# Performance work log

Hardware: AMD Instinct MI355X
Metric: run time of the kernel (lower is better)

## Reference

```python
import jax, jax.numpy as jnp
import numpy as np

N_QUBITS = 6
N_SHARED_LAYERS = 3
N_TASK_LAYERS = 2
ENC_HIDDEN = 256
INPUT_DIM = 784
BATCH = 256
P1Q = 0.001  # 1-qubit depolarizing prob
P2Q = 0.01   # 2-qubit-gate depolarizing approximation (applied as 1q channel, as in source)

C = jnp.complex64
PX = jnp.array([[0, 1], [1, 0]], C)
PY = jnp.array([[0, -1j], [1j, 0]], C)
PZ = jnp.array([[1, 0], [0, -1]], C)
CNOT = jnp.array([[1, 0, 0, 0], [0, 1, 0, 0], [0, 0, 0, 1], [0, 0, 1, 0]], C)

_LOW = 'abcdefghijklmnopqrstuvwxyz'


def _apply(dm, G, axes, batched):
    # contract gate G (rows=out, cols=in) into dm along absolute dm axes `axes`
    k = len(axes)
    G = G.reshape(G.shape[:G.ndim - 2] + (2,) * (2 * k))
    nd = dm.ndim - 1  # 2 * n_qubits
    dm_sub = ['Z'] + list(_LOW[:nd])
    out_sub = list(dm_sub)
    new = 'ABCD'
    gout, gin = [], []
    for j, ax in enumerate(axes):
        gout.append(new[j]); gin.append(dm_sub[ax]); out_sub[ax] = new[j]
    g_str = ('Z' if batched else '') + ''.join(gout) + ''.join(gin)
    return jnp.einsum(f"{g_str},{''.join(dm_sub)}->{''.join(out_sub)}", G, dm)


def apply_unitary(dm, U, wires, n, batched=False):
    # rho -> U rho U^dagger; ket axes are 1+w, bra axes 1+n+w
    dm = _apply(dm, U, [1 + w for w in wires], batched)
    return _apply(dm, jnp.conj(U), [1 + n + w for w in wires], batched)


def depolarize(dm, p, q, n):
    x = apply_unitary(dm, PX, [q], n)
    y = apply_unitary(dm, PY, [q], n)
    z = apply_unitary(dm, PZ, [q], n)
    return (1.0 - p) * dm + (p / 3.0) * (x + y + z)


def rot_mat(phi, theta, omega):
    # PennyLane Rot(phi, theta, omega) = RZ(omega) RY(theta) RZ(phi)
    c = jnp.cos(theta / 2)
    s = jnp.sin(theta / 2)
    ep = jnp.exp(-0.5j * (phi + omega))  # e^{-i(phi+omega)/2}
    em = jnp.exp(0.5j * (phi - omega))   # e^{+i(phi-omega)/2}
    return jnp.stack([jnp.stack([ep * c, -em * s]),
                      jnp.stack([jnp.conj(em) * s, jnp.conj(ep) * c])]).astype(C)


def ry_batched(theta):
    # theta: (B,) -> (B,2,2)
    c = jnp.cos(theta / 2)
    s = jnp.sin(theta / 2)
    return jnp.stack([jnp.stack([c, -s], -1),
                      jnp.stack([s, c], -1)], -2).astype(C)


def strongly_entangling(dm, w, n):
    # PennyLane StronglyEntanglingLayers, default ranges r = (l % (n-1)) + 1, CNOT ring
    L = w.shape[0]
    for l in range(L):
        for i in range(n):
            dm = apply_unitary(dm, rot_mat(w[l, i, 0], w[l, i, 1], w[l, i, 2]), [i], n)
        r = (l % (n - 1)) + 1
        for i in range(n):
            dm = apply_unitary(dm, CNOT, [i, (i + r) % n], n)
    return dm


def circuit(z, shared_w, task_w):
    n = N_QUBITS
    Bz = z.shape[0]
    dm = jnp.zeros((Bz,) + (2,) * (2 * n), C).at[(slice(None),) + (0,) * (2 * n)].set(1.0)
    for i in range(n):
        dm = apply_unitary(dm, ry_batched(z[:, i] * jnp.pi), [i], n, batched=True)
        dm = depolarize(dm, P1Q, i, n)
    dm = strongly_entangling(dm, shared_w, n)
    for i in range(n):
        dm = depolarize(dm, P1Q, i, n)
    for i in range(n - 1):
        dm = depolarize(dm, P2Q, i, n)
    dm = strongly_entangling(dm, task_w, n)
    for i in range(n):
        dm = depolarize(dm, P1Q, i, n)
    D = 2 ** n
    probs = jnp.real(jnp.diagonal(dm.reshape(Bz, D, D), axis1=1, axis2=2))  # (B, D)
    bits = (jnp.arange(D)[:, None] >> jnp.arange(n - 1, -1, -1)[None, :]) & 1  # wire 0 = MSB
    signs = (1 - 2 * bits).astype(jnp.float32)  # (D, n)
    return probs.astype(jnp.float32) @ signs    # (B, n) = <Z_i>


def setup_inputs():
    key = jax.random.key(0)
    ks = jax.random.split(key, 8)
    f = jnp.float32
    return {
        "x": jax.random.normal(ks[0], (BATCH, INPUT_DIM), f),
        "W1": jax.random.normal(ks[1], (ENC_HIDDEN, INPUT_DIM), f) * 0.03,
        "b1": jnp.zeros((ENC_HIDDEN,), f),
        "ln_g": jnp.ones((ENC_HIDDEN,), f),
        "ln_b": jnp.zeros((ENC_HIDDEN,), f),
        "W2": jax.random.normal(ks[2], (N_QUBITS, ENC_HIDDEN), f) * 0.05,
        "b2": jnp.zeros((N_QUBITS,), f),
        "shared_w": jax.random.normal(ks[3], (N_SHARED_LAYERS, N_QUBITS, 3), f) * 0.1,
        "task_w": jax.random.normal(ks[4], (N_TASK_LAYERS, N_QUBITS, 3), f) * 0.1,
        "Wp": jax.random.normal(ks[5], (2, N_QUBITS), f) * 0.1,
        "bp": jnp.zeros((2,), f),
    }


def reference(x, W1, b1, ln_g, ln_b, W2, b2, shared_w, task_w, Wp, bp):
    # encoder: Linear -> ReLU -> LayerNorm -> Linear -> Tanh
    h = jnp.maximum(x @ W1.T + b1, 0.0)
    mu = h.mean(-1, keepdims=True)
    var = ((h - mu) ** 2).mean(-1, keepdims=True)
    h = (h - mu) / jnp.sqrt(var + 1e-5) * ln_g + ln_b
    z = jnp.tanh(h @ W2.T + b2)            # (B, N_QUBITS)
    ev = circuit(z, shared_w, task_w)      # (B, N_QUBITS)
    return ev @ Wp.T + bp                  # (B, 2)
```

## Files before the change

### kernel.cpp

```cpp
#include <hip/hip_runtime.h>
#include <math.h>

#define NQ 6
#define BLK 1024
#define HID 256
#define INDIM 784
#define KC 56
#define NSPLIT 14

#define PW1 0.001f
#define PW2 0.01f
constexpr float WO1 = 1.f - 4.f * PW1 / 3.f;
constexpr float WO2 = 1.f - 4.f * PW2 / 3.f;
constexpr float WOc = WO1 * WO2;

struct alignas(16) RingTabs { int t[3][4096]; };
constexpr RingTabs make_ring_tabs() {
    RingTabs R{};
    for (int ri = 0; ri < 3; ++ri) {
        int r = ri + 1;
        for (int v = 0; v < 4096; ++v) {
            int x[6], z[6];
            for (int w = 0; w < 6; ++w) { x[w] = (v >> (2 * w + 1)) & 1; z[w] = (v >> (2 * w)) & 1; }
            int sgn = 0;
            for (int i = 5; i >= 0; --i) {
                int c = i, tg = (i + r) % 6;
                sgn ^= x[c] & z[tg] & (x[tg] ^ z[c] ^ 1);
                x[tg] ^= x[c];
                z[c]  ^= z[tg];
            }
            int s = 0;
            for (int w = 0; w < 6; ++w) s |= (x[w] << (2 * w + 1)) | (z[w] << (2 * w));
            R.t[ri][v] = s | (sgn << 31);
        }
    }
    return R;
}
static __device__ const RingTabs RT = make_ring_tabs();

__device__ __forceinline__ int swz(int n) {
    return n ^ ((((n >> 6) ^ (n >> 10)) & 3) << 3);
}

template<int CTRL>
__device__ __forceinline__ float qb(float v) {
    int r = __builtin_amdgcn_update_dpp(0, __builtin_bit_cast(int, v), CTRL, 0xF, 0xF, true);
    return __builtin_bit_cast(float, r);
}
template<int OFF>
__device__ __forceinline__ float swzl(float v) {
    return __builtin_bit_cast(float, __builtin_amdgcn_ds_swizzle(__builtin_bit_cast(int, v), OFF));
}

__device__ __forceinline__ void rot_reg(float e[4], float4 rZ, float4 rX, float4 rY) {
    float X = e[2], Y = e[3], Z = e[1];
    e[2] = fmaf(rX.x, X, fmaf(rX.y, Y, rX.z * Z));
    e[3] = fmaf(rY.x, X, fmaf(rY.y, Y, rY.z * Z));
    e[1] = fmaf(rZ.x, X, fmaf(rZ.y, Y, rZ.z * Z));
}
__device__ __forceinline__ void rot_q1(float e[4], float4 cf) {
    #pragma unroll
    for (int j = 0; j < 4; ++j) {
        float vZ = qb<0x55>(e[j]);
        float vX = qb<0xAA>(e[j]);
        float vY = qb<0xFF>(e[j]);
        e[j] = fmaf(cf.x, vX, fmaf(cf.y, vY, fmaf(cf.z, vZ, cf.w * e[j])));
    }
}
__device__ __forceinline__ void rot_q2(float e[4], float4 cf) {
    #pragma unroll
    for (int j = 0; j < 4; ++j) {
        float vZ = swzl<0x093>(e[j]);
        float vX = swzl<0x113>(e[j]);
        float vY = swzl<0x193>(e[j]);
        e[j] = fmaf(cf.x, vX, fmaf(cf.y, vY, fmaf(cf.z, vZ, cf.w * e[j])));
    }
}
__device__ __forceinline__ void rot_q3(float e[4], float4 cf, int lane) {
    int s1 = (lane & 15) | 16, s2 = (lane & 15) | 32, s3 = (lane & 15) | 48;
    #pragma unroll
    for (int j = 0; j < 4; ++j) {
        float vZ = __shfl(e[j], s1, 64);
        float vX = __shfl(e[j], s2, 64);
        float vY = __shfl(e[j], s3, 64);
        e[j] = fmaf(cf.x, vX, fmaf(cf.y, vY, fmaf(cf.z, vZ, cf.w * e[j])));
    }
}

__global__ __launch_bounds__(256)
void enc_gemm(const float* __restrict__ x, const float* __restrict__ W1,
              float* __restrict__ hp)
{
    __shared__ float xsT[KC][64];
    __shared__ float wsT[KC][64];
    const int tid = threadIdx.x;
    const int bid = blockIdx.x;
    const int tile = bid / NSPLIT;
    const int s = bid - tile * NSPLIT;
    const int bb = (tile >> 2) * 64;
    const int bu = (tile & 3) * 64;
    const int k0 = s * KC;

    for (int i = tid; i < 1792; i += 256) {
        int r = i & 63;
        int cb = i >> 6;
        int m = (cb >= 14);
        int c = cb - m * 14;
        const float* src = m ? (W1 + (size_t)(bu + r) * INDIM + k0 + 4 * c)
                             : (x  + (size_t)(bb + r) * INDIM + k0 + 4 * c);
        float4 v = *(const float4*)src;
        float (*dst)[64] = m ? wsT : xsT;
        dst[4 * c + 0][r] = v.x;
        dst[4 * c + 1][r] = v.y;
        dst[4 * c + 2][r] = v.z;
        dst[4 * c + 3][r] = v.w;
    }
    __syncthreads();

    const int tx = tid & 15, ty = tid >> 4;
    float acc[4][4] = {};
    #pragma unroll 7
    for (int k = 0; k < KC; ++k) {
        float4 xv = *(const float4*)&xsT[k][4 * ty];
        float4 wv = *(const float4*)&wsT[k][4 * tx];
        const float xa[4] = {xv.x, xv.y, xv.z, xv.w};
        const float wa[4] = {wv.x, wv.y, wv.z, wv.w};
        #pragma unroll
        for (int i = 0; i < 4; ++i)
            #pragma unroll
            for (int j = 0; j < 4; ++j)
                acc[i][j] = fmaf(xa[i], wa[j], acc[i][j]);
    }
    float* o = hp + (size_t)s * 65536 + (size_t)(bb + 4 * ty) * 256 + bu + 4 * tx;
    #pragma unroll
    for (int i = 0; i < 4; ++i)
        *(float4*)(o + (size_t)i * 256) = make_float4(acc[i][0], acc[i][1], acc[i][2], acc[i][3]);
}

__global__ __launch_bounds__(BLK)
void nqm_kernel(const float* __restrict__ hp, const float* __restrict__ b1,
                const float* __restrict__ ln_g, const float* __restrict__ ln_b,
                const float* __restrict__ W2, const float* __restrict__ b2,
                const float* __restrict__ shared_w, const float* __restrict__ task_w,
                const float* __restrict__ Wp, const float* __restrict__ bp,
                float* __restrict__ out)
{
    __shared__ __align__(16) float dmA[4096];
    __shared__ __align__(16) float dmB[4096];
    __shared__ __align__(16) float4 Mlane[30][4];
    __shared__ float bloch[NQ][4];
    __shared__ float red[4], red2[4];
    __shared__ float zpart[4][8];
    __shared__ float bcast[2];
    __shared__ float evs[8];

    const int tid = threadIdx.x;
    const int b = blockIdx.x;
    const int wv = tid >> 6;
    const int lane = tid & 63;

    float h = 0.0f;
    if (tid < 256) {
        const float* hb = hp + (size_t)b * 256 + tid;
        h = b1[tid];
        #pragma unroll
        for (int s = 0; s < NSPLIT; ++s) h += hb[(size_t)s * 65536];
        h = fmaxf(h, 0.0f);
        float s = h, s2 = h * h;
        #pragma unroll
        for (int off = 32; off > 0; off >>= 1) {
            s  += __shfl_down(s, off, 64);
            s2 += __shfl_down(s2, off, 64);
        }
        if (lane == 0) { red[tid >> 6] = s; red2[tid >> 6] = s2; }
    }
    __syncthreads();
    if (tid == 0) {
        float ts  = red[0] + red[1] + red[2] + red[3];
        float ts2 = red2[0] + red2[1] + red2[2] + red2[3];
        float mu  = ts * (1.0f / HID);
        float var = ts2 * (1.0f / HID) - mu * mu;
        bcast[0] = mu;
        bcast[1] = rsqrtf(var + 1e-5f);
    }
    __syncthreads();
    if (tid < 256) {
        float hnj = (h - bcast[0]) * bcast[1] * ln_g[tid] + ln_b[tid];
        float p[NQ];
        #pragma unroll
        for (int i = 0; i < NQ; ++i) p[i] = hnj * W2[i * HID + tid];
        #pragma unroll
        for (int off = 32; off > 0; off >>= 1) {
            #pragma unroll
            for (int i = 0; i < NQ; ++i) p[i] += __shfl_down(p[i], off, 64);
        }
        if (lane == 0) {
            #pragma unroll
            for (int i = 0; i < NQ; ++i) zpart[tid >> 6][i] = p[i];
        }
    }
    __syncthreads();

    if (tid < NQ) {
        float z = zpart[0][tid] + zpart[1][tid] + zpart[2][tid] + zpart[3][tid] + b2[tid];
        z = tanhf(z);
        float sn, c;
        sincosf(z * 3.14159265358979323846f, &sn, &c);
        bloch[tid][0] = 1.0f;
        bloch[tid][1] = WO1 * c;
        bloch[tid][2] = WO1 * sn;
        bloch[tid][3] = 0.0f;
    } else if (tid < 36) {
        int g = tid - NQ;
        int layer = g / NQ;
        int wire = g % NQ;
        const float* w = (layer < 3) ? (shared_w + (layer * NQ + wire) * 3)
                                     : (task_w + ((layer - 3) * NQ + wire) * 3);
        float phi = w[0], theta = w[1], omega = w[2];
        float sf, cf_, st, ct, so, co;
        sincosf(phi, &sf, &cf_);
        sincosf(theta, &st, &ct);
        sincosf(omega, &so, &co);
        float M00 = co * ct * cf_ - so * sf;
        float M01 = -co * ct * sf - so * cf_;
        float M02 = co * st;
        float M10 = so * ct * cf_ + co * sf;
        float M11 = -so * ct * sf + co * cf_;
        float M12 = so * st;
        float M20 = -st * cf_;
        float M21 = st * sf;
        float M22 = ct;
        float f = (layer == 3) ? ((wire < 5) ? WOc : WO1) : 1.0f;
        Mlane[g][0] = make_float4(0.f, 0.f, 0.f, 1.f);
        Mlane[g][1] = make_float4(f * M20, f * M21, f * M22, 0.f);
        Mlane[g][2] = make_float4(f * M00, f * M01, f * M02, 0.f);
        Mlane[g][3] = make_float4(f * M10, f * M11, f * M12, 0.f);
    }

    const int q1 = lane & 3, q2 = (lane >> 2) & 3, q3 = (lane >> 4) & 3;
    const int q4 = wv & 3, q5 = wv >> 2;
    const int baseB = ((lane & 3) << 10) | (wv << 4) | (lane >> 2);
    const int rtab[4] = {0, 1, 2, 0};
    __syncthreads();

    for (int l = 0; l < 5; ++l) {
        const int g0 = l * 6;
        float e[4];

        if (l == 0) {
            float A = bloch[1][q1] * bloch[2][q2] * bloch[3][q3] * bloch[4][q4] * bloch[5][q5];
            e[0] = A * bloch[0][0];
            e[1] = A * bloch[0][1];
            e[2] = A * bloch[0][2];
            e[3] = A * bloch[0][3];
        } else {
            const int4 te = *(const int4*)&RT.t[rtab[l - 1]][tid << 2];
            float v0 = dmA[swz(te.x & 4095)];
            float v1 = dmA[swz(te.y & 4095)];
            float v2 = dmA[swz(te.z & 4095)];
            float v3 = dmA[swz(te.w & 4095)];
            e[0] = __int_as_float(__float_as_int(v0) ^ (te.x & 0x80000000));
            e[1] = __int_as_float(__float_as_int(v1) ^ (te.y & 0x80000000));
            e[2] = __int_as_float(__float_as_int(v2) ^ (te.z & 0x80000000));
            e[3] = __int_as_float(__float_as_int(v3) ^ (te.w & 0x80000000));
        }
        rot_reg(e, Mlane[g0 + 0][1], Mlane[g0 + 0][2], Mlane[g0 + 0][3]);
        rot_q1(e, Mlane[g0 + 1][q1]);
        rot_q2(e, Mlane[g0 + 2][q2]);
        rot_q3(e, Mlane[g0 + 3][q3], lane);
        *(float4*)&dmB[swz(tid << 2)] = make_float4(e[0], e[1], e[2], e[3]);
        __syncthreads();

        e[0] = dmB[swz(baseB)];
        e[1] = dmB[swz(baseB + 256)];
        e[2] = dmB[swz(baseB + 512)];
        e[3] = dmB[swz(baseB + 768)];
        rot_reg(e, Mlane[g0 + 4][1], Mlane[g0 + 4][2], Mlane[g0 + 4][3]);
        rot_q1(e, Mlane[g0 + 5][lane & 3]);
        dmA[swz(baseB)]       = e[0];
        dmA[swz(baseB + 256)] = e[1];
        dmA[swz(baseB + 512)] = e[2];
        dmA[swz(baseB + 768)] = e[3];
        __syncthreads();
    }

    if (tid < NQ) {
        int e = RT.t[1][1 << (2 * tid)];
        float v = dmA[swz(e & 4095)];
        v = __int_as_float(__float_as_int(v) ^ (e & 0x80000000));
        evs[tid] = WO1 * v;
    }
    __syncthreads();
    if (tid < 2) {
        float o = bp[tid];
        #pragma unroll
        for (int i = 0; i < NQ; ++i) o = fmaf(evs[i], Wp[tid * NQ + i], o);
        out[b * 2 + tid] = o;
    }
}

extern "C" void kernel_launch(void* const* d_in, const int* in_sizes, int n_in,
                              void* d_out, int out_size, void* d_ws, size_t ws_size,
                              hipStream_t stream) {
    (void)in_sizes; (void)n_in; (void)ws_size; (void)out_size;
    const float* x        = (const float*)d_in[0];
    const float* W1       = (const float*)d_in[1];
    const float* b1       = (const float*)d_in[2];
    const float* ln_g     = (const float*)d_in[3];
    const float* ln_b     = (const float*)d_in[4];
    const float* W2       = (const float*)d_in[5];
    const float* b2       = (const float*)d_in[6];
    const float* shared_w = (const float*)d_in[7];
    const float* task_w   = (const float*)d_in[8];
    const float* Wp       = (const float*)d_in[9];
    const float* bp       = (const float*)d_in[10];
    float* out = (float*)d_out;
    float* hp  = (float*)d_ws;

    hipLaunchKernelGGL(enc_gemm, dim3(16 * NSPLIT), dim3(256), 0, stream, x, W1, hp);
    hipLaunchKernelGGL(nqm_kernel, dim3(256), dim3(BLK), 0, stream,
                       hp, b1, ln_g, ln_b, W2, b2, shared_w, task_w, Wp, bp, out);
}
```

Baseline: 95.25 us.

## Fuse encoder GEMM and circuit kernels into one cooperative launch with grid sync

Merges the split-K encoder GEMM and the density-matrix circuit kernel into a single cooperative kernel of 256 blocks of 1024 threads. The first 224 blocks compute the GEMM partials with a 2x2 per-thread tile, then a grid-wide sync orders them before the circuit phase. Shared memory is overlapped through a union. The swizzle is also folded into the constexpr ring tables, saving runtime index math. This removes one kernel launch and its inter-kernel gap, but adds grid-sync cost, a lower-ILP GEMM tile, and needs all 256 large blocks to be co-resident.

```diff
diff --git a/kernel.cpp b/kernel.cpp
--- a/kernel.cpp
+++ b/kernel.cpp
@@ -1,5 +1,8 @@
 #include <hip/hip_runtime.h>
+#include <hip/hip_cooperative_groups.h>
 #include <math.h>
+
+namespace cg = cooperative_groups;
 
 #define NQ 6
 #define BLK 1024
@@ -13,6 +16,13 @@
 constexpr float WO1 = 1.f - 4.f * PW1 / 3.f;
 constexpr float WO2 = 1.f - 4.f * PW2 / 3.f;
 constexpr float WOc = WO1 * WO2;
+
+constexpr int cswz(int n) {
+    return n ^ ((((n >> 6) ^ (n >> 10)) & 3) << 3);
+}
+__device__ __forceinline__ int swz(int n) {
+    return n ^ ((((n >> 6) ^ (n >> 10)) & 3) << 3);
+}
 
 struct alignas(16) RingTabs { int t[3][4096]; };
 constexpr RingTabs make_ring_tabs() {
@@ -31,16 +41,12 @@
             }
             int s = 0;
             for (int w = 0; w < 6; ++w) s |= (x[w] << (2 * w + 1)) | (z[w] << (2 * w));
-            R.t[ri][v] = s | (sgn << 31);
+            R.t[ri][v] = cswz(s) | (sgn << 31);
         }
     }
     return R;
 }
 static __device__ const RingTabs RT = make_ring_tabs();
-
-__device__ __forceinline__ int swz(int n) {
-    return n ^ ((((n >> 6) ^ (n >> 10)) & 3) << 3);
-}
 
 template<int CTRL>
 __device__ __forceinline__ float qb(float v) {
@@ -87,78 +93,79 @@
     }
 }
 
-__global__ __launch_bounds__(256)
-void enc_gemm(const float* __restrict__ x, const float* __restrict__ W1,
-              float* __restrict__ hp)
+union SharedU {
+    struct {
+        float xsT[KC][64];
+        float wsT[KC][64];
+    } g;
+    struct {
+        alignas(16) float dmA[4096];
+        alignas(16) float dmB[4096];
+        alignas(16) float4 Mlane[30][4];
+        float bloch[NQ][4];
+        float red[4], red2[4];
+        float zpart[4][8];
+        float bcast[2];
+        float evs[8];
+    } c;
+};
+
+__global__ __launch_bounds__(BLK)
+void fused_k(const float* __restrict__ x, const float* __restrict__ W1,
+             const float* __restrict__ b1, const float* __restrict__ ln_g,
+             const float* __restrict__ ln_b, const float* __restrict__ W2,
+             const float* __restrict__ b2, const float* __restrict__ shared_w,
+             const float* __restrict__ task_w, const float* __restrict__ Wp,
+             const float* __restrict__ bp, float* __restrict__ out,
+             float* __restrict__ hp)
 {
-    __shared__ float xsT[KC][64];
-    __shared__ float wsT[KC][64];
-    const int tid = threadIdx.x;
-    const int bid = blockIdx.x;
-    const int tile = bid / NSPLIT;
-    const int s = bid - tile * NSPLIT;
-    const int bb = (tile >> 2) * 64;
-    const int bu = (tile & 3) * 64;
-    const int k0 = s * KC;
-
-    for (int i = tid; i < 1792; i += 256) {
-        int r = i & 63;
-        int cb = i >> 6;
-        int m = (cb >= 14);
-        int c = cb - m * 14;
-        const float* src = m ? (W1 + (size_t)(bu + r) * INDIM + k0 + 4 * c)
-                             : (x  + (size_t)(bb + r) * INDIM + k0 + 4 * c);
-        float4 v = *(const float4*)src;
-        float (*dst)[64] = m ? wsT : xsT;
-        dst[4 * c + 0][r] = v.x;
-        dst[4 * c + 1][r] = v.y;
-        dst[4 * c + 2][r] = v.z;
-        dst[4 * c + 3][r] = v.w;
-    }
-    __syncthreads();
-
-    const int tx = tid & 15, ty = tid >> 4;
-    float acc[4][4] = {};
-    #pragma unroll 7
-    for (int k = 0; k < KC; ++k) {
-        float4 xv = *(const float4*)&xsT[k][4 * ty];
-        float4 wv = *(const float4*)&wsT[k][4 * tx];
-        const float xa[4] = {xv.x, xv.y, xv.z, xv.w};
-        const float wa[4] = {wv.x, wv.y, wv.z, wv.w};
-        #pragma unroll
-        for (int i = 0; i < 4; ++i)
-            #pragma unroll
-            for (int j = 0; j < 4; ++j)
-                acc[i][j] = fmaf(xa[i], wa[j], acc[i][j]);
-    }
-    float* o = hp + (size_t)s * 65536 + (size_t)(bb + 4 * ty) * 256 + bu + 4 * tx;
-    #pragma unroll
-    for (int i = 0; i < 4; ++i)
-        *(float4*)(o + (size_t)i * 256) = make_float4(acc[i][0], acc[i][1], acc[i][2], acc[i][3]);
-}
-
-__global__ __launch_bounds__(BLK)
-void nqm_kernel(const float* __restrict__ hp, const float* __restrict__ b1,
-                const float* __restrict__ ln_g, const float* __restrict__ ln_b,
-                const float* __restrict__ W2, const float* __restrict__ b2,
-                const float* __restrict__ shared_w, const float* __restrict__ task_w,
-                const float* __restrict__ Wp, const float* __restrict__ bp,
-                float* __restrict__ out)
-{
-    __shared__ __align__(16) float dmA[4096];
-    __shared__ __align__(16) float dmB[4096];
-    __shared__ __align__(16) float4 Mlane[30][4];
-    __shared__ float bloch[NQ][4];
-    __shared__ float red[4], red2[4];
-    __shared__ float zpart[4][8];
-    __shared__ float bcast[2];
-    __shared__ float evs[8];
-
+    __shared__ SharedU su;
     const int tid = threadIdx.x;
     const int b = blockIdx.x;
     const int wv = tid >> 6;
     const int lane = tid & 63;
 
+    if (b < 16 * NSPLIT) {
+        const int tile = b / NSPLIT;
+        const int s = b - tile * NSPLIT;
+        const int bb = (tile >> 2) * 64;
+        const int bu = (tile & 3) * 64;
+        const int k0 = s * KC;
+
+        for (int i = tid; i < 1792; i += BLK) {
+            int r = i & 63;
+            int cb = i >> 6;
+            int m = (cb >= 14);
+            int c = cb - m * 14;
+            const float* src = m ? (W1 + (size_t)(bu + r) * INDIM + k0 + 4 * c)
+                                 : (x  + (size_t)(bb + r) * INDIM + k0 + 4 * c);
+            float4 v = *(const float4*)src;
+            float (*dst)[64] = m ? su.g.wsT : su.g.xsT;
+            dst[4 * c + 0][r] = v.x;
+            dst[4 * c + 1][r] = v.y;
+            dst[4 * c + 2][r] = v.z;
+            dst[4 * c + 3][r] = v.w;
+        }
+        __syncthreads();
+
+        const int tx = tid & 31, ty = tid >> 5;
+        float a00 = 0.f, a01 = 0.f, a10 = 0.f, a11 = 0.f;
+        #pragma unroll 7
+        for (int k = 0; k < KC; ++k) {
+            float2 xv = *(const float2*)&su.g.xsT[k][2 * ty];
+            float2 wvv = *(const float2*)&su.g.wsT[k][2 * tx];
+            a00 = fmaf(xv.x, wvv.x, a00);
+            a01 = fmaf(xv.x, wvv.y, a01);
+            a10 = fmaf(xv.y, wvv.x, a10);
+            a11 = fmaf(xv.y, wvv.y, a11);
+        }
+        float* o = hp + (size_t)s * 65536 + (size_t)(bb + 2 * ty) * 256 + bu + 2 * tx;
+        o[0] = a00; o[1] = a01;
+        o[256] = a10; o[257] = a11;
+    }
+
+    cg::this_grid().sync();
+
     float h = 0.0f;
     if (tid < 256) {
         const float* hb = hp + (size_t)b * 256 + tid;
@@ -172,20 +179,20 @@
             s  += __shfl_down(s, off, 64);
             s2 += __shfl_down(s2, off, 64);
         }
-        if (lane == 0) { red[tid >> 6] = s; red2[tid >> 6] = s2; }
+        if (lane == 0) { su.c.red[tid >> 6] = s; su.c.red2[tid >> 6] = s2; }
     }
     __syncthreads();
     if (tid == 0) {
-        float ts  = red[0] + red[1] + red[2] + red[3];
-        float ts2 = red2[0] + red2[1] + red2[2] + red2[3];
+        float ts  = su.c.red[0] + su.c.red[1] + su.c.red[2] + su.c.red[3];
+        float ts2 = su.c.red2[0] + su.c.red2[1] + su.c.red2[2] + su.c.red2[3];
         float mu  = ts * (1.0f / HID);
         float var = ts2 * (1.0f / HID) - mu * mu;
-        bcast[0] = mu;
-        bcast[1] = rsqrtf(var + 1e-5f);
+        su.c.bcast[0] = mu;
+        su.c.bcast[1] = rsqrtf(var + 1e-5f);
     }
     __syncthreads();
     if (tid < 256) {
-        float hnj = (h - bcast[0]) * bcast[1] * ln_g[tid] + ln_b[tid];
+        float hnj = (h - su.c.bcast[0]) * su.c.bcast[1] * ln_g[tid] + ln_b[tid];
         float p[NQ];
         #pragma unroll
         for (int i = 0; i < NQ; ++i) p[i] = hnj * W2[i * HID + tid];
@@ -196,20 +203,21 @@
         }
         if (lane == 0) {
             #pragma unroll
-            for (int i = 0; i < NQ; ++i) zpart[tid >> 6][i] = p[i];
+            for (int i = 0; i < NQ; ++i) su.c.zpart[tid >> 6][i] = p[i];
         }
     }
     __syncthreads();
 
     if (tid < NQ) {
-        float z = zpart[0][tid] + zpart[1][tid] + zpart[2][tid] + zpart[3][tid] + b2[tid];
+        float z = su.c.zpart[0][tid] + su.c.zpart[1][tid] + su.c.zpart[2][tid]
+                + su.c.zpart[3][tid] + b2[tid];
         z = tanhf(z);
         float sn, c;
         sincosf(z * 3.14159265358979323846f, &sn, &c);
-        bloch[tid][0] = 1.0f;
-        bloch[tid][1] = WO1 * c;
-        bloch[tid][2] = WO1 * sn;
-        bloch[tid][3] = 0.0f;
+        su.c.bloch[tid][0] = 1.0f;
+        su.c.bloch[tid][1] = WO1 * c;
+        su.c.bloch[tid][2] = WO1 * sn;
+        su.c.bloch[tid][3] = 0.0f;
     } else if (tid < 36) {
         int g = tid - NQ;
         int layer = g / NQ;
@@ -231,10 +239,10 @@
         float M21 = st * sf;
         float M22 = ct;
         float f = (layer == 3) ? ((wire < 5) ? WOc : WO1) : 1.0f;
-        Mlane[g][0] = make_float4(0.f, 0.f, 0.f, 1.f);
-        Mlane[g][1] = make_float4(f * M20, f * M21, f * M22, 0.f);
-        Mlane[g][2] = make_float4(f * M00, f * M01, f * M02, 0.f);
-        Mlane[g][3] = make_float4(f * M10, f * M11, f * M12, 0.f);
+        su.c.Mlane[g][0] = make_float4(0.f, 0.f, 0.f, 1.f);
+        su.c.Mlane[g][1] = make_float4(f * M20, f * M21, f * M22, 0.f);
+        su.c.Mlane[g][2] = make_float4(f * M00, f * M01, f * M02, 0.f);
+        su.c.Mlane[g][3] = make_float4(f * M10, f * M11, f * M12, 0.f);
     }
 
     const int q1 = lane & 3, q2 = (lane >> 2) & 3, q3 = (lane >> 4) & 3;
@@ -248,53 +256,54 @@
         float e[4];
 
         if (l == 0) {
-            float A = bloch[1][q1] * bloch[2][q2] * bloch[3][q3] * bloch[4][q4] * bloch[5][q5];
-            e[0] = A * bloch[0][0];
-            e[1] = A * bloch[0][1];
-            e[2] = A * bloch[0][2];
-            e[3] = A * bloch[0][3];
+            float A = su.c.bloch[1][q1] * su.c.bloch[2][q2] * su.c.bloch[3][q3]
+                    * su.c.bloch[4][q4] * su.c.bloch[5][q5];
+            e[0] = A * su.c.bloch[0][0];
+            e[1] = A * su.c.bloch[0][1];
+            e[2] = A * su.c.bloch[0][2];
+            e[3] = A * su.c.bloch[0][3];
         } else {
             const int4 te = *(const int4*)&RT.t[rtab[l - 1]][tid << 2];
-            float v0 = dmA[swz(te.x & 4095)];
-            float v1 = dmA[swz(te.y & 4095)];
-            float v2 = dmA[swz(te.z & 4095)];
-            float v3 = dmA[swz(te.w & 4095)];
+            float v0 = su.c.dmA[te.x & 4095];
+            float v1 = su.c.dmA[te.y & 4095];
+            float v2 = su.c.dmA[te.z & 4095];
+            float v3 = su.c.dmA[te.w & 4095];
             e[0] = __int_as_float(__float_as_int(v0) ^ (te.x & 0x80000000));
             e[1] = __int_as_float(__float_as_int(v1) ^ (te.y & 0x80000000));
             e[2] = __int_as_float(__float_as_int(v2) ^ (te.z & 0x80000000));
             e[3] = __int_as_float(__float_as_int(v3) ^ (te.w & 0x80000000));
         }
-        rot_reg(e, Mlane[g0 + 0][1], Mlane[g0 + 0][2], Mlane[g0 + 0][3]);
-        rot_q1(e, Mlane[g0 + 1][q1]);
-        rot_q2(e, Mlane[g0 + 2][q2]);
-        rot_q3(e, Mlane[g0 + 3][q3], lane);
-        *(float4*)&dmB[swz(tid << 2)] = make_float4(e[0], e[1], e[2], e[3]);
+        rot_reg(e, su.c.Mlane[g0 + 0][1], su.c.Mlane[g0 + 0][2], su.c.Mlane[g0 + 0][3]);
+        rot_q1(e, su.c.Mlane[g0 + 1][q1]);
+        rot_q2(e, su.c.Mlane[g0 + 2][q2]);
+        rot_q3(e, su.c.Mlane[g0 + 3][q3], lane);
+        *(float4*)&su.c.dmB[swz(tid << 2)] = make_float4(e[0], e[1], e[2], e[3]);
         __syncthreads();
 
-        e[0] = dmB[swz(baseB)];
-        e[1] = dmB[swz(baseB + 256)];
-        e[2] = dmB[swz(baseB + 512)];
-        e[3] = dmB[swz(baseB + 768)];
-        rot_reg(e, Mlane[g0 + 4][1], Mlane[g0 + 4][2], Mlane[g0 + 4][3]);
-        rot_q1(e, Mlane[g0 + 5][lane & 3]);
-        dmA[swz(baseB)]       = e[0];
-        dmA[swz(baseB + 256)] = e[1];
-        dmA[swz(baseB + 512)] = e[2];
-        dmA[swz(baseB + 768)] = e[3];
+        e[0] = su.c.dmB[swz(baseB)];
+        e[1] = su.c.dmB[swz(baseB + 256)];
+        e[2] = su.c.dmB[swz(baseB + 512)];
+        e[3] = su.c.dmB[swz(baseB + 768)];
+        rot_reg(e, su.c.Mlane[g0 + 4][1], su.c.Mlane[g0 + 4][2], su.c.Mlane[g0 + 4][3]);
+        rot_q1(e, su.c.Mlane[g0 + 5][lane & 3]);
+        su.c.dmA[swz(baseB)]       = e[0];
+        su.c.dmA[swz(baseB + 256)] = e[1];
+        su.c.dmA[swz(baseB + 512)] = e[2];
+        su.c.dmA[swz(baseB + 768)] = e[3];
         __syncthreads();
     }
 
     if (tid < NQ) {
         int e = RT.t[1][1 << (2 * tid)];
-        float v = dmA[swz(e & 4095)];
+        float v = su.c.dmA[e & 4095];
         v = __int_as_float(__float_as_int(v) ^ (e & 0x80000000));
-        evs[tid] = WO1 * v;
+        su.c.evs[tid] = WO1 * v;
     }
     __syncthreads();
     if (tid < 2) {
         float o = bp[tid];
         #pragma unroll
-        for (int i = 0; i < NQ; ++i) o = fmaf(evs[i], Wp[tid * NQ + i], o);
+        for (int i = 0; i < NQ; ++i) o = fmaf(su.c.evs[i], Wp[tid * NQ + i], o);
         out[b * 2 + tid] = o;
     }
 }
@@ -317,7 +326,9 @@
     float* out = (float*)d_out;
     float* hp  = (float*)d_ws;
 
-    hipLaunchKernelGGL(enc_gemm, dim3(16 * NSPLIT), dim3(256), 0, stream, x, W1, hp);
-    hipLaunchKernelGGL(nqm_kernel, dim3(256), dim3(BLK), 0, stream,
-                       hp, b1, ln_g, ln_b, W2, b2, shared_w, task_w, Wp, bp, out);
-}
+    void* args[] = {(void*)&x, (void*)&W1, (void*)&b1, (void*)&ln_g, (void*)&ln_b,
+                    (void*)&W2, (void*)&b2, (void*)&shared_w, (void*)&task_w,
+                    (void*)&Wp, (void*)&bp, (void*)&out, (void*)&hp};
+    hipLaunchCooperativeKernel((const void*)fused_k, dim3(256), dim3(BLK),
+                               args, 0, stream);
+}
```

Measured after the change: 148.0 us. 55.4% more time.
